# Kernel optimization log

Measured on AMD Instinct MI355X. Metric: run time of the kernel, lower is better.

Reference implementation:

```python
import jax, jax.numpy as jnp
import numpy as np

B, C, Himg, Wimg = 8, 256, 128, 128
KC, VC, HID = 256, 256, 1024


def _conv(x, w, b, pad, groups=1):
    y = jax.lax.conv_general_dilated(
        x, w, (1, 1), [(pad[0], pad[0]), (pad[1], pad[1])],
        dimension_numbers=('NCHW', 'OIHW', 'NCHW'), feature_group_count=groups)
    return y + b[None, :, None, None]


def _ln(x, g, b, eps=1e-5):
    m = x.mean(-1, keepdims=True)
    v = ((x - m) ** 2).mean(-1, keepdims=True)
    return (x - m) / jnp.sqrt(v + eps) * g + b


def setup_inputs() -> dict:
    key = jax.random.key(0)
    ks = jax.random.split(key, 24)
    s = 0.02
    inp = {
        'x': jax.random.normal(ks[0], (B, C, Himg, Wimg), jnp.float32),
        'H': Himg, 'W': Wimg,
        # directional K/Q convs: dir0 kernel (1,3), dir1 kernel (3,1)
        'wk1': s * jax.random.normal(ks[1], (KC, C, 1, 3), jnp.float32),
        'bk1': jnp.zeros((KC,), jnp.float32),
        'wk2': s * jax.random.normal(ks[2], (KC, C, 3, 1), jnp.float32),
        'bk2': jnp.zeros((KC,), jnp.float32),
        'wq1': s * jax.random.normal(ks[3], (KC, C, 1, 3), jnp.float32),
        'bq1': jnp.zeros((KC,), jnp.float32),
        'wq2': s * jax.random.normal(ks[4], (KC, C, 3, 1), jnp.float32),
        'bq2': jnp.zeros((KC,), jnp.float32),
        'wv': s * jax.random.normal(ks[5], (VC, C, 1, 1), jnp.float32),
        'bv': jnp.zeros((VC,), jnp.float32),
        'wr': s * jax.random.normal(ks[6], (C, 2 * VC, 1, 1), jnp.float32),
        'br': jnp.zeros((C,), jnp.float32),
        'g1': jnp.ones((C,), jnp.float32), 'b1': jnp.zeros((C,), jnp.float32),
        'g2': jnp.ones((C,), jnp.float32), 'b2': jnp.zeros((C,), jnp.float32),
        'w_fc1': s * jax.random.normal(ks[7], (HID, C), jnp.float32),
        'b_fc1': jnp.zeros((HID,), jnp.float32),
        'w_dw': s * jax.random.normal(ks[8], (HID, 1, 3, 3), jnp.float32),
        'b_dw': jnp.zeros((HID,), jnp.float32),
        'w_fc2': s * jax.random.normal(ks[9], (C, HID), jnp.float32),
        'b_fc2': jnp.zeros((C,), jnp.float32),
    }
    return inp


def reference(x, H, W, wk1, bk1, wk2, bk2, wq1, bq1, wq2, bq2, wv, bv, wr, br,
              g1, b1, g2, b2, w_fc1, b_fc1, w_dw, b_dw, w_fc2, b_fc2):
    b, c, h, w = x.shape
    N = h * w
    xseq = x.reshape(b, c, N).transpose(0, 2, 1)          # b N c
    n1 = _ln(xseq, g1, b1)
    xn = n1.transpose(0, 2, 1).reshape(b, c, h, w)

    val = _conv(xn, wv, bv, (0, 0)).reshape(b, VC, N)     # b vc n
    attended, maps = [], []
    ctx = None
    for (wk, bk, wq, bq, pad) in [(wk1, bk1, wq1, bq1, (0, 1)),
                                  (wk2, bk2, wq2, bq2, (1, 0))]:
        k = _conv(xn, wk, bk, pad).reshape(b, KC, N)
        q = _conv(xn, wq, bq, pad).reshape(b, KC, N)
        key_s = jax.nn.softmax(k, axis=2)                 # softmax over spatial
        qry_s = jax.nn.softmax(q, axis=1)                 # softmax over channels
        ctx = jnp.einsum('bkn,bvn->bkv', key_s, val)      # O(n) linear attention
        av = jnp.einsum('bkv,bkn->bvn', ctx, qry_s).reshape(b, VC, h, w)
        attended.append(av)
        maps.append(key_s.mean(axis=1).reshape(b, h, w))
    agg = jnp.concatenate(attended, axis=1)               # b 2vc h w
    attn = _conv(agg, wr, br, (0, 0))                     # b c h w
    amap = jnp.stack(maps, axis=0).mean(axis=0)

    tx = xseq + attn.reshape(b, c, N).transpose(0, 2, 1)  # residual
    n2 = _ln(tx, g2, b2)
    h1 = n2 @ w_fc1.T + b_fc1                             # b N 4c
    h1img = h1.transpose(0, 2, 1).reshape(b, HID, h, w)
    dw = _conv(h1img, w_dw, b_dw, (1, 1), groups=HID)
    a = jax.nn.gelu(dw.reshape(b, HID, N).transpose(0, 2, 1), approximate=False)
    ffn = a @ w_fc2.T + b_fc2
    mx = (tx + ffn).transpose(0, 2, 1).reshape(b, c, h, w)
    return (mx, ctx, amap)
```

## Files before the change

kernel.cpp:

```cpp
#include <hip/hip_runtime.h>
#include <hip/hip_bf16.h>

#define B_ 8
#define C_ 256
#define H_ 128
#define W_ 128
#define N_ 16384
#define KC_ 256
#define VC_ 256
#define HID_ 1024

typedef unsigned short ushort_t;
typedef __bf16 bf16x8 __attribute__((ext_vector_type(8)));
typedef float f32x4 __attribute__((ext_vector_type(4)));
typedef ushort_t u16x8 __attribute__((ext_vector_type(8)));

static __device__ __forceinline__ ushort_t f2bu(float f) {
  __hip_bfloat16 h = __float2bfloat16(f);
  return *reinterpret_cast<ushort_t*>(&h);
}
static __device__ __forceinline__ float bu2f(ushort_t u) {
  __hip_bfloat16 h;
  *reinterpret_cast<ushort_t*>(&h) = u;
  return __bfloat162float(h);
}

#define GLD16(gp, lp) __builtin_amdgcn_global_load_lds( \
    (const __attribute__((address_space(1))) void*)(gp), \
    (__attribute__((address_space(3))) void*)(lp), 16, 0, 0)

__global__ __launch_bounds__(256) void pack_all(
    const float* __restrict__ wk1, const float* __restrict__ wk2,
    const float* __restrict__ wq1, const float* __restrict__ wq2,
    const float* __restrict__ wv, const float* __restrict__ wfc1,
    const float* __restrict__ wfc2, const float* __restrict__ wdw,
    const float* __restrict__ bk1, const float* __restrict__ bk2,
    const float* __restrict__ bq1, const float* __restrict__ bq2,
    const float* __restrict__ wr,
    ushort_t* __restrict__ zbuf, float* __restrict__ fzero,
    float* __restrict__ bK, float* __restrict__ bQ, float* __restrict__ wdwT,
    ushort_t* __restrict__ wvp, ushort_t* __restrict__ wfc1p,
    ushort_t* __restrict__ wfc2p, ushort_t* __restrict__ wrp,
    ushort_t* __restrict__ wkkp, ushort_t* __restrict__ wqqp) {
  int idx = blockIdx.x * 256 + threadIdx.x;
  const int MC = KC_ * C_;
  if (idx < 512) {
    zbuf[idx] = 0; fzero[idx] = 0.f;
    bK[idx] = (idx < 256) ? bk1[idx] : bk2[idx - 256];
    bQ[idx] = (idx < 256) ? bq1[idx] : bq2[idx - 256];
    return;
  }
  idx -= 512;
  if (idx < 9216) { int c = idx / 9, t = idx % 9; wdwT[t * HID_ + c] = wdw[idx]; return; }
  idx -= 9216;
  if (idx < VC_ * C_) { wvp[idx] = f2bu(wv[idx]); return; }
  idx -= VC_ * C_;
  if (idx < HID_ * C_) { wfc1p[idx] = f2bu(wfc1[idx]); return; }
  idx -= HID_ * C_;
  if (idx < C_ * HID_) { wfc2p[idx] = f2bu(wfc2[idx]); return; }
  idx -= C_ * HID_;
  if (idx < C_ * 512) { wrp[idx] = f2bu(wr[idx]); return; }
  idx -= C_ * 512;
  if (idx < MC) {
    #pragma unroll
    for (int t = 0; t < 3; ++t) wkkp[t * MC + idx] = f2bu(wk1[idx * 3 + t]);
    return;
  }
  idx -= MC;
  if (idx < MC) {
    #pragma unroll
    for (int t = 0; t < 3; ++t) wkkp[3 * MC + t * MC + idx] = f2bu(wk2[idx * 3 + t]);
    return;
  }
  idx -= MC;
  if (idx < MC) {
    #pragma unroll
    for (int t = 0; t < 3; ++t) wqqp[t * MC + idx] = f2bu(wq1[idx * 3 + t]);
    return;
  }
  idx -= MC;
  if (idx < MC) {
    #pragma unroll
    for (int t = 0; t < 3; ++t) wqqp[3 * MC + t * MC + idx] = f2bu(wq2[idx * 3 + t]);
    return;
  }
}

__global__ __launch_bounds__(256) void ln1t_kernel(const float* __restrict__ x,
    const float* __restrict__ g, const float* __restrict__ beta,
    ushort_t* __restrict__ out) {
  __shared__ float T[256][67];
  __shared__ float st[2][4][64];
  __shared__ float mr[64], rs[64];
  int z = blockIdx.z;
  int n0 = blockIdx.x * 64;
  int t = threadIdx.x;
  const float* xb = x + (size_t)z * C_ * N_;
  #pragma unroll
  for (int j = 0; j < 16; ++j) {
    int e = (j * 256 + t) * 4;
    int c = e >> 6, n = e & 63;
    float4 v = *(const float4*)&xb[(size_t)c * N_ + n0 + n];
    T[c][n] = v.x; T[c][n + 1] = v.y; T[c][n + 2] = v.z; T[c][n + 3] = v.w;
  }
  __syncthreads();
  {
    int n = t & 63, part = t >> 6;
    float s1 = 0.f, s2 = 0.f;
    for (int c = part * 64; c < part * 64 + 64; ++c) { float v = T[c][n]; s1 += v; s2 += v * v; }
    st[0][part][n] = s1; st[1][part][n] = s2;
  }
  __syncthreads();
  if (t < 64) {
    float s1 = st[0][0][t] + st[0][1][t] + st[0][2][t] + st[0][3][t];
    float s2 = st[1][0][t] + st[1][1][t] + st[1][2][t] + st[1][3][t];
    float m = s1 * (1.f / C_);
    float v = s2 * (1.f / C_) - m * m;
    mr[t] = m; rs[t] = rsqrtf(v + 1e-5f);
  }
  __syncthreads();
  {
    int n = t >> 2, cc = (t & 3) * 64;
    float m = mr[n], r = rs[n];
    ushort_t* po = out + (size_t)z * N_ * C_ + (size_t)(n0 + n) * C_ + cc;
    #pragma unroll
    for (int j0 = 0; j0 < 64; j0 += 8) {
      u16x8 o;
      #pragma unroll
      for (int j = 0; j < 8; ++j) {
        int c = cc + j0 + j;
        o[j] = f2bu((T[c][n] - m) * r * g[c] + beta[c]);
      }
      *(u16x8*)(po + j0) = o;
    }
  }
}

__global__ __launch_bounds__(256) void ln2t_kernel(const ushort_t* __restrict__ x,
    const float* __restrict__ g, const float* __restrict__ beta,
    ushort_t* __restrict__ out) {
  __shared__ ushort_t T[256][72];
  __shared__ float st[2][4][64];
  __shared__ float mr[64], rs[64];
  int z = blockIdx.z;
  int n0 = blockIdx.x * 64;
  int t = threadIdx.x;
  const ushort_t* xb = x + (size_t)z * C_ * N_;
  #pragma unroll
  for (int j = 0; j < 8; ++j) {
    int e = (j * 256 + t) * 8;
    int c = e >> 6, n = e & 63;
    *(u16x8*)&T[c][n] = *(const u16x8*)&xb[(size_t)c * N_ + n0 + n];
  }
  __syncthreads();
  {
    int n = t & 63, part = t >> 6;
    float s1 = 0.f, s2 = 0.f;
    for (int c = part * 64; c < part * 64 + 64; ++c) { float v = bu2f(T[c][n]); s1 += v; s2 += v * v; }
    st[0][part][n] = s1; st[1][part][n] = s2;
  }
  __syncthreads();
  if (t < 64) {
    float s1 = st[0][0][t] + st[0][1][t] + st[0][2][t] + st[0][3][t];
    float s2 = st[1][0][t] + st[1][1][t] + st[1][2][t] + st[1][3][t];
    float m = s1 * (1.f / C_);
    float v = s2 * (1.f / C_) - m * m;
    mr[t] = m; rs[t] = rsqrtf(v + 1e-5f);
  }
  __syncthreads();
  {
    int n = t >> 2, cc = (t & 3) * 64;
    float m = mr[n], r = rs[n];
    ushort_t* po = out + (size_t)z * N_ * C_ + (size_t)(n0 + n) * C_ + cc;
    #pragma unroll
    for (int j0 = 0; j0 < 64; j0 += 8) {
      u16x8 o;
      #pragma unroll
      for (int j = 0; j < 8; ++j) {
        int c = cc + j0 + j;
        o[j] = f2bu((bu2f(T[c][n]) - m) * r * g[c] + beta[c]);
      }
      *(u16x8*)(po + j0) = o;
    }
  }
}

template<int TAPS, int DIMSEL, int OMODE, int SPLIT, bool BDUAL>
__global__ __launch_bounds__(256) void mfma_gemm(
    const ushort_t* __restrict__ A, long Abatch, int lda, long Aplane, long Adirstride,
    const ushort_t* __restrict__ B, const ushort_t* __restrict__ B2, long Bbatch, int ldb,
    const float* __restrict__ bias,
    const float* __restrict__ resF, const ushort_t* __restrict__ resB, long Resbatch,
    float* __restrict__ outF, ushort_t* __restrict__ outB, ushort_t* __restrict__ outB2,
    long Outbatch, int ldo, int Ksteps, const ushort_t* __restrict__ zbuf) {
  __shared__ ushort_t sm[17408];
  int tid = threadIdx.x;
  int bx = blockIdx.x, by = blockIdx.y, bz = blockIdx.z;
  if (gridDim.x == 128) bx = ((bx & 7) << 4) | (bx >> 3);
  int b = bz / SPLIT, sK = bz % SPLIT;
  long koff = (long)sK * Ksteps * 64;
  int dsel = (DIMSEL == 3) ? (by < 2 ? 1 : 2) : DIMSEL;
  int m0 = (DIMSEL == 3) ? ((by & 1) * 128) : (by * 128);
  int bofs = (DIMSEL == 3) ? ((by >> 1) * 256) : 0;
  const ushort_t* Ab = A + (size_t)b * Abatch + koff + ((DIMSEL == 3) ? (long)(by >> 1) * Adirstride : 0L);
  const ushort_t* Bb = B + (size_t)b * Bbatch + (BDUAL ? 0 : koff);
  const ushort_t* B2b = BDUAL ? (B2 + (size_t)b * Bbatch) : nullptr;
  int n0 = bx * 128;
  int lane = tid & 63, wid = tid >> 6, wm = wid >> 1, wn = wid & 1;

  f32x4 acc[4][4];
  #pragma unroll
  for (int i = 0; i < 4; i++)
    #pragma unroll
    for (int j = 0; j < 4; j++) acc[i][j] = (f32x4)0.f;

  for (int t = 0; t < TAPS; ++t) {
    if (TAPS == 3 && dsel == 2) {
      if ((bx == 0 && t == 0) || (bx == H_ - 1 && t == 2)) continue;
    }
    const ushort_t* At = Ab + (long)t * Aplane;
    for (int ks = 0; ks < Ksteps; ++ks) {
      int k0 = ks * 64;
      #pragma unroll
      for (int i = 0; i < 4; i++) {
        int s = tid + i * 256;
        int row = s >> 3, pc = s & 7;
        int lc = pc ^ (row & 7);
        const ushort_t* g = At + (long)(m0 + row) * lda + k0 + lc * 8;
        GLD16(g, &sm[s * 8]);
      }
      #pragma unroll
      for (int i = 0; i < 4; i++) {
        int s = tid + i * 256;
        int row = s >> 3, pc = s & 7;
        int lc = pc ^ (row & 7);
        const ushort_t* g;
        if (BDUAL) {
          const ushort_t* Bsel = (ks < Ksteps / 2) ? Bb : B2b;
          int kb = ((ks < Ksteps / 2) ? ks : ks - Ksteps / 2) * 64;
          g = Bsel + (long)(n0 + row) * ldb + kb + lc * 8;
        } else if (TAPS == 3 && dsel == 1) {
          int wpos = row + (t - 1);
          if (0 <= wpos && wpos < W_)
            g = Bb + (long)(n0 + row + (t - 1)) * ldb + k0 + lc * 8;
          else
            g = zbuf;
        } else if (TAPS == 3 && dsel == 2) {
          g = Bb + (long)(n0 + row + (t - 1) * W_) * ldb + k0 + lc * 8;
        } else {
          g = Bb + (long)(n0 + row) * ldb + k0 + lc * 8;
        }
        GLD16(g, &sm[8192 + s * 8]);
      }
      __syncthreads();
      #pragma unroll
      for (int kk = 0; kk < 2; kk++) {
        bf16x8 av[4], bv[4];
        int r16 = lane & 15;
        int sl = (lane >> 4) + kk * 4;
        #pragma unroll
        for (int fm = 0; fm < 4; fm++) {
          int row = wm * 64 + fm * 16 + r16;
          av[fm] = *(const bf16x8*)&sm[row * 64 + ((sl ^ (row & 7)) * 8)];
        }
        #pragma unroll
        for (int fn = 0; fn < 4; fn++) {
          int row = wn * 64 + fn * 16 + r16;
          bv[fn] = *(const bf16x8*)&sm[8192 + row * 64 + ((sl ^ (row & 7)) * 8)];
        }
        #pragma unroll
        for (int fm = 0; fm < 4; fm++)
          #pragma unroll
          for (int fn = 0; fn < 4; fn++)
            acc[fm][fn] = __builtin_amdgcn_mfma_f32_16x16x32_bf16(av[fm], bv[fn], acc[fm][fn], 0, 0, 0);
      }
      __syncthreads();
    }
  }

  int r16 = lane & 15, rq = lane >> 4;
  if (OMODE == 1 || OMODE == 2 || OMODE == 7) {
    ushort_t* obase = (DIMSEL == 3 && blockIdx.y >= 2) ? outB2 : outB;
    ushort_t* ob = obase + (size_t)bz * Outbatch;
    #pragma unroll
    for (int fm = 0; fm < 4; fm++) {
      #pragma unroll
      for (int fn = 0; fn < 4; fn++) {
        int lm = wm * 64 + fm * 16 + rq * 4;
        int ln = wn * 64 + fn * 16 + r16;
        f32x4 a = acc[fm][fn];
        if (OMODE == 2) {
          #pragma unroll
          for (int r = 0; r < 4; r++)
            sm[ln * 136 + lm + r] = f2bu(a[r] + bias[bofs + m0 + lm + r]);
        } else {
          #pragma unroll
          for (int r = 0; r < 4; r++)
            sm[(lm + r) * 136 + ln] = f2bu(a[r] + bias[bofs + m0 + lm + r]);
        }
      }
    }
    __syncthreads();
    int row = tid >> 1, half = (tid & 1) * 64;
    const ushort_t* src = &sm[row * 136 + half];
    if (OMODE == 7) {
      const float* xb = resF + (size_t)bz * Resbatch + (size_t)(m0 + row) * ldo + n0 + half;
      ushort_t* dst = &ob[(size_t)(m0 + row) * ldo + n0 + half];
      #pragma unroll
      for (int j = 0; j < 8; j++) {
        u16x8 v = *(const u16x8*)(src + j * 8);
        float4 x0 = *(const float4*)(xb + j * 8);
        float4 x1 = *(const float4*)(xb + j * 8 + 4);
        u16x8 o;
        o[0] = f2bu(bu2f(v[0]) + x0.x); o[1] = f2bu(bu2f(v[1]) + x0.y);
        o[2] = f2bu(bu2f(v[2]) + x0.z); o[3] = f2bu(bu2f(v[3]) + x0.w);
        o[4] = f2bu(bu2f(v[4]) + x1.x); o[5] = f2bu(bu2f(v[5]) + x1.y);
        o[6] = f2bu(bu2f(v[6]) + x1.z); o[7] = f2bu(bu2f(v[7]) + x1.w);
        *(u16x8*)(dst + j * 8) = o;
      }
    } else {
      ushort_t* dst;
      if (OMODE == 1) dst = &ob[(size_t)(m0 + row) * ldo + n0 + half];
      else            dst = &ob[(size_t)(n0 + row) * ldo + m0 + half];
      #pragma unroll
      for (int j = 0; j < 8; j++)
        *(u16x8*)(dst + j * 8) = *(const u16x8*)(src + j * 8);
    }
  } else {
    #pragma unroll
    for (int fm = 0; fm < 4; fm++) {
      #pragma unroll
      for (int fn = 0; fn < 4; fn++) {
        int mrow = m0 + wm * 64 + fm * 16 + rq * 4;
        int ncol = n0 + wn * 64 + fn * 16 + r16;
        f32x4 a = acc[fm][fn];
        if (OMODE == 6) {
          float* of = outF + (size_t)bz * Outbatch;
          #pragma unroll
          for (int r = 0; r < 4; r++)
            of[(size_t)(mrow + r) * ldo + ncol] = a[r];
        } else if (OMODE == 8) {
          float* of = outF + (size_t)bz * Outbatch;
          const ushort_t* rp = resB + (size_t)bz * Resbatch;
          #pragma unroll
          for (int r = 0; r < 4; r++) {
            size_t o = (size_t)(mrow + r) * ldo + ncol;
            of[o] = a[r] + bias[mrow + r] + bu2f(rp[o]);
          }
        }
      }
    }
  }
}

__global__ __launch_bounds__(256) void softmax_spatial2(ushort_t* __restrict__ p0,
                                                        ushort_t* __restrict__ p1) {
  int r = blockIdx.x;
  ushort_t* p = (r < B_ * KC_) ? (p0 + (size_t)r * N_) : (p1 + (size_t)(r - B_ * KC_) * N_);
  int tid = threadIdx.x;
  __shared__ float red[256];
  u16x8 v[8];
  #pragma unroll
  for (int j = 0; j < 8; j++) v[j] = *(const u16x8*)&p[tid * 8 + j * 2048];
  float mx = -1e30f;
  #pragma unroll
  for (int j = 0; j < 8; j++)
    #pragma unroll
    for (int e = 0; e < 8; e++) mx = fmaxf(mx, bu2f(v[j][e]));
  red[tid] = mx; __syncthreads();
  for (int s = 128; s > 0; s >>= 1) { if (tid < s) red[tid] = fmaxf(red[tid], red[tid + s]); __syncthreads(); }
  mx = red[0]; __syncthreads();
  float sum = 0.f;
  #pragma unroll
  for (int j = 0; j < 8; j++)
    #pragma unroll
    for (int e = 0; e < 8; e++) sum += __expf(bu2f(v[j][e]) - mx);
  red[tid] = sum; __syncthreads();
  for (int s = 128; s > 0; s >>= 1) { if (tid < s) red[tid] += red[tid + s]; __syncthreads(); }
  float inv = 1.f / red[0];
  #pragma unroll
  for (int j = 0; j < 8; j++) {
    u16x8 o;
    #pragma unroll
    for (int e = 0; e < 8; e++) o[e] = f2bu(__expf(bu2f(v[j][e]) - mx) * inv);
    *(u16x8*)&p[tid * 8 + j * 2048] = o;
  }
}

__global__ __launch_bounds__(256) void softmax_channel2(ushort_t* __restrict__ p0,
                                                        ushort_t* __restrict__ p1) {
  int tid = threadIdx.x;
  size_t rowg = (size_t)blockIdx.x * 64 + (tid >> 2);
  int part = tid & 3;
  ushort_t* q = (rowg < (size_t)B_ * N_) ? (p0 + rowg * KC_)
                                         : (p1 + (rowg - (size_t)B_ * N_) * KC_);
  ushort_t* qp = q + part * 64;
  u16x8 v[8];
  #pragma unroll
  for (int j = 0; j < 8; j++) v[j] = *(const u16x8*)&qp[j * 8];
  float mx = -1e30f;
  #pragma unroll
  for (int j = 0; j < 8; j++)
    #pragma unroll
    for (int e = 0; e < 8; e++) mx = fmaxf(mx, bu2f(v[j][e]));
  mx = fmaxf(mx, __shfl_xor(mx, 1));
  mx = fmaxf(mx, __shfl_xor(mx, 2));
  float sum = 0.f;
  #pragma unroll
  for (int j = 0; j < 8; j++)
    #pragma unroll
    for (int e = 0; e < 8; e++) sum += __expf(bu2f(v[j][e]) - mx);
  sum += __shfl_xor(sum, 1);
  sum += __shfl_xor(sum, 2);
  float inv = 1.f / sum;
  #pragma unroll
  for (int j = 0; j < 8; j++) {
    u16x8 o;
    #pragma unroll
    for (int e = 0; e < 8; e++) o[e] = f2bu(__expf(bu2f(v[j][e]) - mx) * inv);
    *(u16x8*)&qp[j * 8] = o;
  }
}

__global__ __launch_bounds__(256) void amap2_kernel(const ushort_t* __restrict__ k0,
    const ushort_t* __restrict__ k1, float* __restrict__ amap) {
  __shared__ float red[256][8];
  int tid = threadIdx.x;
  int ngrp = tid & 63, part = tid >> 6;
  int nblock = blockIdx.x * 512;
  int b = nblock >> 14;
  int n = (nblock & 16383) + ngrp * 8;
  const ushort_t* b0 = k0 + (size_t)b * KC_ * N_ + n;
  const ushort_t* b1 = k1 + (size_t)b * KC_ * N_ + n;
  float s[8];
  #pragma unroll
  for (int j = 0; j < 8; j++) s[j] = 0.f;
  for (int c = part * 64; c < part * 64 + 64; ++c) {
    u16x8 a = *(const u16x8*)&b0[(size_t)c * N_];
    u16x8 d = *(const u16x8*)&b1[(size_t)c * N_];
    #pragma unroll
    for (int j = 0; j < 8; j++) s[j] += bu2f(a[j]) + bu2f(d[j]);
  }
  #pragma unroll
  for (int j = 0; j < 8; j++) red[tid][j] = s[j];
  __syncthreads();
  if (tid < 64) {
    float t[8];
    #pragma unroll
    for (int j = 0; j < 8; j++)
      t[j] = (red[tid][j] + red[tid + 64][j] + red[tid + 128][j] + red[tid + 192][j])
             * (1.f / (2.f * KC_));
    float* dst = amap + (size_t)nblock + tid * 8;
    *(float4*)dst = make_float4(t[0], t[1], t[2], t[3]);
    *(float4*)(dst + 4) = make_float4(t[4], t[5], t[6], t[7]);
  }
}

template<bool F32OUT>
__global__ __launch_bounds__(256) void ctx_reduce(const float* __restrict__ part,
                                                  float* __restrict__ outF,
                                                  ushort_t* __restrict__ outB, int split) {
  int idx = blockIdx.x * 256 + threadIdx.x;
  int b = idx >> 16;
  int r = idx & 65535;
  float s = 0.f;
  for (int k = 0; k < split; k++)
    s += part[((size_t)(b * split + k)) * KC_ * VC_ + r];
  if (F32OUT) outF[idx] = s;
  outB[idx] = f2bu(s);
}

__global__ __launch_bounds__(256) void dwgelu_t(const ushort_t* __restrict__ h1t,
    const float* __restrict__ wdwT, const float* __restrict__ bdw,
    ushort_t* __restrict__ actT) {
  int pix = blockIdx.x * 2 + (threadIdx.x >> 7);
  int c = (threadIdx.x & 127) * 8;
  int h = pix >> 7, w = pix & 127;
  float s[8];
  {
    float4 b0 = *(const float4*)&bdw[c];
    float4 b1 = *(const float4*)&bdw[c + 4];
    s[0]=b0.x; s[1]=b0.y; s[2]=b0.z; s[3]=b0.w;
    s[4]=b1.x; s[5]=b1.y; s[6]=b1.z; s[7]=b1.w;
  }
  #pragma unroll
  for (int di = -1; di <= 1; ++di) {
    int h2 = h + di;
    if ((unsigned)h2 >= H_) continue;
    #pragma unroll
    for (int dj = -1; dj <= 1; ++dj) {
      int w2 = w + dj;
      if ((unsigned)w2 >= W_) continue;
      int tap = (di + 1) * 3 + (dj + 1);
      u16x8 v = *(const u16x8*)&h1t[(size_t)(h2 * W_ + w2) * HID_ + c];
      const float* wp = &wdwT[tap * HID_ + c];
      float4 w0 = *(const float4*)wp, w1 = *(const float4*)(wp + 4);
      s[0] += w0.x * bu2f(v[0]); s[1] += w0.y * bu2f(v[1]);
      s[2] += w0.z * bu2f(v[2]); s[3] += w0.w * bu2f(v[3]);
      s[4] += w1.x * bu2f(v[4]); s[5] += w1.y * bu2f(v[5]);
      s[6] += w1.z * bu2f(v[6]); s[7] += w1.w * bu2f(v[7]);
    }
  }
  u16x8 o;
  #pragma unroll
  for (int j = 0; j < 8; j++) {
    float gl = 0.5f * s[j] * (1.f + erff(s[j] * 0.70710678118654752f));
    o[j] = f2bu(gl);
  }
  *(u16x8*)&actT[(size_t)pix * HID_ + c] = o;
}

extern "C" void kernel_launch(void* const* d_in, const int* in_sizes, int n_in,
                              void* d_out, int out_size, void* d_ws, size_t ws_size,
                              hipStream_t stream) {
  const float* x    = (const float*)d_in[0];
  const float* wk1  = (const float*)d_in[3];
  const float* bk1  = (const float*)d_in[4];
  const float* wk2  = (const float*)d_in[5];
  const float* bk2  = (const float*)d_in[6];
  const float* wq1  = (const float*)d_in[7];
  const float* bq1  = (const float*)d_in[8];
  const float* wq2  = (const float*)d_in[9];
  const float* bq2  = (const float*)d_in[10];
  const float* wv   = (const float*)d_in[11];
  const float* bv   = (const float*)d_in[12];
  const float* wr   = (const float*)d_in[13];
  const float* br   = (const float*)d_in[14];
  const float* g1   = (const float*)d_in[15];
  const float* b1   = (const float*)d_in[16];
  const float* g2   = (const float*)d_in[17];
  const float* b2   = (const float*)d_in[18];
  const float* wfc1 = (const float*)d_in[19];
  const float* bfc1 = (const float*)d_in[20];
  const float* wdw  = (const float*)d_in[21];
  const float* bdw  = (const float*)d_in[22];
  const float* wfc2 = (const float*)d_in[23];
  const float* bfc2 = (const float*)d_in[24];

  const size_t big = (size_t)B_ * C_ * N_;
  const long  CN  = (long)C_ * N_;
  const long  NC2 = (long)N_ * C_;

  uint8_t* w8 = (uint8_t*)d_ws;
  size_t off = 0;
  ushort_t* xnt  = (ushort_t*)(w8 + off); off += 67108864;
  ushort_t* kq   = (ushort_t*)(w8 + off); off += 67108864;
  ushort_t* Mbuf = (ushort_t*)(w8 + off); off += (size_t)B_ * C_ * 512 * 2;
  ushort_t* wkkp = (ushort_t*)(w8 + off); off += 6 * KC_ * C_ * 2;
  ushort_t* wqqp = (ushort_t*)(w8 + off); off += 6 * KC_ * C_ * 2;
  ushort_t* wvp  = (ushort_t*)(w8 + off); off += VC_ * C_ * 2;
  ushort_t* wfc1p= (ushort_t*)(w8 + off); off += HID_ * C_ * 2;
  ushort_t* wfc2p= (ushort_t*)(w8 + off); off += C_ * HID_ * 2;
  float* wdwT    = (float*)(w8 + off);    off += 9 * HID_ * 4;
  float* bK      = (float*)(w8 + off);    off += 512 * 4;
  float* bQ      = (float*)(w8 + off);    off += 512 * 4;
  float* fzero   = (float*)(w8 + off);    off += 512 * 4;
  ushort_t* wrp  = (ushort_t*)(w8 + off); off += C_ * 512 * 2;
  ushort_t* ctx0b= (ushort_t*)(w8 + off); off += (size_t)B_ * KC_ * VC_ * 2;
  ushort_t* ctx1b= (ushort_t*)(w8 + off); off += (size_t)B_ * KC_ * VC_ * 2;
  ushort_t* zbuf = (ushort_t*)(w8 + off); off += 1024;
  float* part    = (float*)(w8 + off);
  size_t need4 = off + (size_t)4 * B_ * KC_ * VC_ * 4;
  size_t need8 = off + (size_t)8 * B_ * KC_ * VC_ * 4;
  int csplit;
  if (ws_size >= need8) csplit = 8;
  else if (ws_size >= need4) csplit = 4;
  else return;

  float* mx_out   = (float*)d_out;
  float* ctx_out  = mx_out + big;
  float* amap_out = ctx_out + (size_t)B_ * KC_ * VC_;

  ushort_t* mxlo = (ushort_t*)d_out;
  ushort_t* mxhi = (ushort_t*)d_out + big;

  ushort_t* txn  = xnt;
  ushort_t* h1t  = kq;
  ushort_t* actT = kq + (size_t)N_ * HID_;

  dim3 blk(256);

  pack_all<<<3878, blk, 0, stream>>>(wk1, wk2, wq1, wq2, wv, wfc1, wfc2, wdw,
                                     bk1, bk2, bq1, bq2, wr,
                                     zbuf, fzero, bK, bQ, wdwT,
                                     wvp, wfc1p, wfc2p, wrp, wkkp, wqqp);

  ln1t_kernel<<<dim3(N_ / 64, 1, B_), blk, 0, stream>>>(x, g1, b1, xnt);

  mfma_gemm<1, 0, 1, 1, false><<<dim3(N_ / 128, VC_ / 128, B_), blk, 0, stream>>>(
      wvp, 0, C_, 0, 0, xnt, nullptr, NC2, C_, bv, nullptr, nullptr, 0,
      nullptr, mxlo, nullptr, (long)VC_ * N_, N_, C_ / 64, zbuf);

  mfma_gemm<3, 3, 1, 1, false><<<dim3(N_ / 128, 4, B_), blk, 0, stream>>>(
      wkkp, 0, C_, (long)KC_ * C_, (long)3 * KC_ * C_, xnt, nullptr, NC2, C_,
      bK, nullptr, nullptr, 0,
      nullptr, kq, mxhi, (long)KC_ * N_, N_, C_ / 64, zbuf);

  softmax_spatial2<<<2 * B_ * KC_, blk, 0, stream>>>(kq, mxhi);
  amap2_kernel<<<B_ * N_ / 512, blk, 0, stream>>>(kq, mxhi, amap_out);

  for (int d = 0; d < 2; ++d) {
    const ushort_t* Ksrc = d ? mxhi : kq;
    if (csplit == 8)
      mfma_gemm<1, 0, 6, 8, false><<<dim3(VC_ / 128, KC_ / 128, B_ * 8), blk, 0, stream>>>(
          Ksrc, (long)KC_ * N_, N_, 0, 0, mxlo, nullptr, (long)VC_ * N_, N_,
          nullptr, nullptr, nullptr, 0,
          part, nullptr, nullptr, (long)KC_ * VC_, VC_, (N_ / 8) / 64, zbuf);
    else
      mfma_gemm<1, 0, 6, 4, false><<<dim3(VC_ / 128, KC_ / 128, B_ * 4), blk, 0, stream>>>(
          Ksrc, (long)KC_ * N_, N_, 0, 0, mxlo, nullptr, (long)VC_ * N_, N_,
          nullptr, nullptr, nullptr, 0,
          part, nullptr, nullptr, (long)KC_ * VC_, VC_, (N_ / 4) / 64, zbuf);
    if (d == 0)
      ctx_reduce<false><<<B_ * KC_ * VC_ / 256, blk, 0, stream>>>(part, nullptr, ctx0b, csplit);
    else
      ctx_reduce<true><<<B_ * KC_ * VC_ / 256, blk, 0, stream>>>(part, ctx_out, ctx1b, csplit);
  }

  mfma_gemm<3, 3, 2, 1, false><<<dim3(N_ / 128, 4, B_), blk, 0, stream>>>(
      wqqp, 0, C_, (long)KC_ * C_, (long)3 * KC_ * C_, xnt, nullptr, NC2, C_,
      bQ, nullptr, nullptr, 0,
      nullptr, kq, mxlo, (long)N_ * KC_, KC_, C_ / 64, zbuf);

  softmax_channel2<<<2 * B_ * N_ / 64, blk, 0, stream>>>(kq, mxlo);

  mfma_gemm<1, 0, 1, 1, false><<<dim3(KC_ / 128, C_ / 128, B_), blk, 0, stream>>>(
      wrp, 0, 512, 0, 0, ctx0b, nullptr, (long)KC_ * VC_, VC_, fzero, nullptr, nullptr, 0,
      nullptr, Mbuf, nullptr, (long)C_ * 512, 512, VC_ / 64, zbuf);
  mfma_gemm<1, 0, 1, 1, false><<<dim3(KC_ / 128, C_ / 128, B_), blk, 0, stream>>>(
      wrp + 256, 0, 512, 0, 0, ctx1b, nullptr, (long)KC_ * VC_, VC_, fzero, nullptr, nullptr, 0,
      nullptr, Mbuf + 256, nullptr, (long)C_ * 512, 512, VC_ / 64, zbuf);

  mfma_gemm<1, 0, 7, 1, true><<<dim3(N_ / 128, C_ / 128, B_), blk, 0, stream>>>(
      Mbuf, (long)C_ * 512, 512, 0, 0, kq, mxlo, (long)N_ * KC_, KC_,
      br, x, nullptr, CN,
      nullptr, mxhi, nullptr, CN, N_, 8, zbuf);

  ln2t_kernel<<<dim3(N_ / 64, 1, B_), blk, 0, stream>>>(mxhi, g2, b2, txn);

  hipMemcpyAsync(part, mxhi + (size_t)7 * CN, (size_t)CN * 2,
                 hipMemcpyDeviceToDevice, stream);

  for (int b = 0; b < B_; ++b) {
    mfma_gemm<1, 0, 2, 1, false><<<dim3(N_ / 128, HID_ / 128, 1), blk, 0, stream>>>(
        wfc1p, 0, C_, 0, 0, txn + (size_t)b * NC2, nullptr, 0, C_,
        bfc1, nullptr, nullptr, 0,
        nullptr, h1t, nullptr, 0, HID_, C_ / 64, zbuf);
    dwgelu_t<<<N_ / 2, blk, 0, stream>>>(h1t, wdwT, bdw, actT);
    const ushort_t* txb = (b == 7) ? (const ushort_t*)part : (mxhi + (size_t)b * CN);
    mfma_gemm<1, 0, 8, 1, false><<<dim3(N_ / 128, C_ / 128, 1), blk, 0, stream>>>(
        wfc2p, 0, HID_, 0, 0, actT, nullptr, 0, HID_,
        bfc2, nullptr, txb, 0,
        mx_out + (size_t)b * CN, nullptr, nullptr, 0, N_, HID_ / 64, zbuf);
  }
}
```

Baseline: 1.481 ms.

## Fuse V projection into directional K conv GEMM and narrow channel softmax rows

Merges the value 1x1 projection into the 3-tap K convolution GEMM launch by adding a DIMSEL=4 mode. The grid grows to six M-blocks, and the last two blocks run a single tap on the V weights, which are laid out right after the K weights, writing to a third output buffer. The change removes one kernel launch and lets the K and V GEMMs share the input tile stream in one grid. Separately, the channel softmax now uses 8 threads per row instead of 4, giving more blocks and interleaved 16-byte accesses. The combined bias buffer and the reused zero buffer replace separate allocations.

```diff
diff --git a/kernel.cpp b/kernel.cpp
--- a/kernel.cpp
+++ b/kernel.cpp
@@ -36,21 +36,25 @@
     const float* __restrict__ wfc2, const float* __restrict__ wdw,
     const float* __restrict__ bk1, const float* __restrict__ bk2,
     const float* __restrict__ bq1, const float* __restrict__ bq2,
-    const float* __restrict__ wr,
-    ushort_t* __restrict__ zbuf, float* __restrict__ fzero,
-    float* __restrict__ bK, float* __restrict__ bQ, float* __restrict__ wdwT,
+    const float* __restrict__ bv, const float* __restrict__ wr,
+    ushort_t* __restrict__ zbuf,
+    float* __restrict__ bKV, float* __restrict__ bQ, float* __restrict__ wdwT,
     ushort_t* __restrict__ wvp, ushort_t* __restrict__ wfc1p,
     ushort_t* __restrict__ wfc2p, ushort_t* __restrict__ wrp,
     ushort_t* __restrict__ wkkp, ushort_t* __restrict__ wqqp) {
   int idx = blockIdx.x * 256 + threadIdx.x;
   const int MC = KC_ * C_;
   if (idx < 512) {
-    zbuf[idx] = 0; fzero[idx] = 0.f;
-    bK[idx] = (idx < 256) ? bk1[idx] : bk2[idx - 256];
+    zbuf[idx] = 0;
     bQ[idx] = (idx < 256) ? bq1[idx] : bq2[idx - 256];
     return;
   }
   idx -= 512;
+  if (idx < 768) {
+    bKV[idx] = (idx < 256) ? bk1[idx] : (idx < 512 ? bk2[idx - 256] : bv[idx - 512]);
+    return;
+  }
+  idx -= 768;
   if (idx < 9216) { int c = idx / 9, t = idx % 9; wdwT[t * HID_ + c] = wdw[idx]; return; }
   idx -= 9216;
   if (idx < VC_ * C_) { wvp[idx] = f2bu(wv[idx]); return; }
@@ -192,6 +196,7 @@
     const float* __restrict__ bias,
     const float* __restrict__ resF, const ushort_t* __restrict__ resB, long Resbatch,
     float* __restrict__ outF, ushort_t* __restrict__ outB, ushort_t* __restrict__ outB2,
+    ushort_t* __restrict__ outB3,
     long Outbatch, int ldo, int Ksteps, const ushort_t* __restrict__ zbuf) {
   __shared__ ushort_t sm[17408];
   int tid = threadIdx.x;
@@ -199,10 +204,13 @@
   if (gridDim.x == 128) bx = ((bx & 7) << 4) | (bx >> 3);
   int b = bz / SPLIT, sK = bz % SPLIT;
   long koff = (long)sK * Ksteps * 64;
-  int dsel = (DIMSEL == 3) ? (by < 2 ? 1 : 2) : DIMSEL;
-  int m0 = (DIMSEL == 3) ? ((by & 1) * 128) : (by * 128);
-  int bofs = (DIMSEL == 3) ? ((by >> 1) * 256) : 0;
-  const ushort_t* Ab = A + (size_t)b * Abatch + koff + ((DIMSEL == 3) ? (long)(by >> 1) * Adirstride : 0L);
+  int dsel = (DIMSEL == 3) ? (by < 2 ? 1 : 2)
+           : (DIMSEL == 4) ? (by < 2 ? 1 : (by < 4 ? 2 : 0))
+           : DIMSEL;
+  int m0 = (DIMSEL == 3 || DIMSEL == 4) ? ((by & 1) * 128) : (by * 128);
+  int bofs = (DIMSEL == 3 || DIMSEL == 4) ? ((by >> 1) * 256) : 0;
+  const ushort_t* Ab = A + (size_t)b * Abatch + koff
+      + ((DIMSEL == 3 || DIMSEL == 4) ? (long)(by >> 1) * Adirstride : 0L);
   const ushort_t* Bb = B + (size_t)b * Bbatch + (BDUAL ? 0 : koff);
   const ushort_t* B2b = BDUAL ? (B2 + (size_t)b * Bbatch) : nullptr;
   int n0 = bx * 128;
@@ -218,7 +226,8 @@
     if (TAPS == 3 && dsel == 2) {
       if ((bx == 0 && t == 0) || (bx == H_ - 1 && t == 2)) continue;
     }
-    const ushort_t* At = Ab + (long)t * Aplane;
+    if (DIMSEL == 4 && dsel == 0 && t != 1) continue;
+    const ushort_t* At = Ab + ((DIMSEL == 4 && dsel == 0) ? 0L : (long)t * Aplane);
     for (int ks = 0; ks < Ksteps; ++ks) {
       int k0 = ks * 64;
       #pragma unroll
@@ -280,7 +289,11 @@
 
   int r16 = lane & 15, rq = lane >> 4;
   if (OMODE == 1 || OMODE == 2 || OMODE == 7) {
-    ushort_t* obase = (DIMSEL == 3 && blockIdx.y >= 2) ? outB2 : outB;
+    ushort_t* obase;
+    if (DIMSEL == 3 || DIMSEL == 4)
+      obase = (blockIdx.y >= 4) ? outB3 : (blockIdx.y >= 2 ? outB2 : outB);
+    else
+      obase = outB;
     ushort_t* ob = obase + (size_t)bz * Outbatch;
     #pragma unroll
     for (int fm = 0; fm < 4; fm++) {
@@ -390,35 +403,36 @@
 __global__ __launch_bounds__(256) void softmax_channel2(ushort_t* __restrict__ p0,
                                                         ushort_t* __restrict__ p1) {
   int tid = threadIdx.x;
-  size_t rowg = (size_t)blockIdx.x * 64 + (tid >> 2);
-  int part = tid & 3;
+  size_t rowg = (size_t)blockIdx.x * 32 + (tid >> 3);
+  int part = tid & 7;
   ushort_t* q = (rowg < (size_t)B_ * N_) ? (p0 + rowg * KC_)
                                          : (p1 + (rowg - (size_t)B_ * N_) * KC_);
-  ushort_t* qp = q + part * 64;
-  u16x8 v[8];
-  #pragma unroll
-  for (int j = 0; j < 8; j++) v[j] = *(const u16x8*)&qp[j * 8];
+  u16x8 v[4];
+  #pragma unroll
+  for (int j = 0; j < 4; j++) v[j] = *(const u16x8*)&q[part * 8 + j * 64];
   float mx = -1e30f;
   #pragma unroll
-  for (int j = 0; j < 8; j++)
+  for (int j = 0; j < 4; j++)
     #pragma unroll
     for (int e = 0; e < 8; e++) mx = fmaxf(mx, bu2f(v[j][e]));
   mx = fmaxf(mx, __shfl_xor(mx, 1));
   mx = fmaxf(mx, __shfl_xor(mx, 2));
+  mx = fmaxf(mx, __shfl_xor(mx, 4));
   float sum = 0.f;
   #pragma unroll
-  for (int j = 0; j < 8; j++)
+  for (int j = 0; j < 4; j++)
     #pragma unroll
     for (int e = 0; e < 8; e++) sum += __expf(bu2f(v[j][e]) - mx);
   sum += __shfl_xor(sum, 1);
   sum += __shfl_xor(sum, 2);
+  sum += __shfl_xor(sum, 4);
   float inv = 1.f / sum;
   #pragma unroll
-  for (int j = 0; j < 8; j++) {
+  for (int j = 0; j < 4; j++) {
     u16x8 o;
     #pragma unroll
     for (int e = 0; e < 8; e++) o[e] = f2bu(__expf(bu2f(v[j][e]) - mx) * inv);
-    *(u16x8*)&qp[j * 8] = o;
+    *(u16x8*)&q[part * 8 + j * 64] = o;
   }
 }
 
@@ -540,21 +554,21 @@
   const size_t big = (size_t)B_ * C_ * N_;
   const long  CN  = (long)C_ * N_;
   const long  NC2 = (long)N_ * C_;
+  const int   MC  = KC_ * C_;
 
   uint8_t* w8 = (uint8_t*)d_ws;
   size_t off = 0;
   ushort_t* xnt  = (ushort_t*)(w8 + off); off += 67108864;
   ushort_t* kq   = (ushort_t*)(w8 + off); off += 67108864;
   ushort_t* Mbuf = (ushort_t*)(w8 + off); off += (size_t)B_ * C_ * 512 * 2;
-  ushort_t* wkkp = (ushort_t*)(w8 + off); off += 6 * KC_ * C_ * 2;
-  ushort_t* wqqp = (ushort_t*)(w8 + off); off += 6 * KC_ * C_ * 2;
-  ushort_t* wvp  = (ushort_t*)(w8 + off); off += VC_ * C_ * 2;
+  ushort_t* wkkp = (ushort_t*)(w8 + off); off += 6 * MC * 2;
+  ushort_t* wvp  = (ushort_t*)(w8 + off); off += MC * 2;
+  ushort_t* wqqp = (ushort_t*)(w8 + off); off += 6 * MC * 2;
   ushort_t* wfc1p= (ushort_t*)(w8 + off); off += HID_ * C_ * 2;
   ushort_t* wfc2p= (ushort_t*)(w8 + off); off += C_ * HID_ * 2;
   float* wdwT    = (float*)(w8 + off);    off += 9 * HID_ * 4;
-  float* bK      = (float*)(w8 + off);    off += 512 * 4;
+  float* bKV     = (float*)(w8 + off);    off += 768 * 4;
   float* bQ      = (float*)(w8 + off);    off += 512 * 4;
-  float* fzero   = (float*)(w8 + off);    off += 512 * 4;
   ushort_t* wrp  = (ushort_t*)(w8 + off); off += C_ * 512 * 2;
   ushort_t* ctx0b= (ushort_t*)(w8 + off); off += (size_t)B_ * KC_ * VC_ * 2;
   ushort_t* ctx1b= (ushort_t*)(w8 + off); off += (size_t)B_ * KC_ * VC_ * 2;
@@ -566,6 +580,7 @@
   if (ws_size >= need8) csplit = 8;
   else if (ws_size >= need4) csplit = 4;
   else return;
+  const float* fzero = (const float*)zbuf;
 
   float* mx_out   = (float*)d_out;
   float* ctx_out  = mx_out + big;
@@ -580,21 +595,17 @@
 
   dim3 blk(256);
 
-  pack_all<<<3878, blk, 0, stream>>>(wk1, wk2, wq1, wq2, wv, wfc1, wfc2, wdw,
-                                     bk1, bk2, bq1, bq2, wr,
-                                     zbuf, fzero, bK, bQ, wdwT,
+  pack_all<<<3881, blk, 0, stream>>>(wk1, wk2, wq1, wq2, wv, wfc1, wfc2, wdw,
+                                     bk1, bk2, bq1, bq2, bv, wr,
+                                     zbuf, bKV, bQ, wdwT,
                                      wvp, wfc1p, wfc2p, wrp, wkkp, wqqp);
 
   ln1t_kernel<<<dim3(N_ / 64, 1, B_), blk, 0, stream>>>(x, g1, b1, xnt);
 
-  mfma_gemm<1, 0, 1, 1, false><<<dim3(N_ / 128, VC_ / 128, B_), blk, 0, stream>>>(
-      wvp, 0, C_, 0, 0, xnt, nullptr, NC2, C_, bv, nullptr, nullptr, 0,
-      nullptr, mxlo, nullptr, (long)VC_ * N_, N_, C_ / 64, zbuf);
-
-  mfma_gemm<3, 3, 1, 1, false><<<dim3(N_ / 128, 4, B_), blk, 0, stream>>>(
-      wkkp, 0, C_, (long)KC_ * C_, (long)3 * KC_ * C_, xnt, nullptr, NC2, C_,
-      bK, nullptr, nullptr, 0,
-      nullptr, kq, mxhi, (long)KC_ * N_, N_, C_ / 64, zbuf);
+  mfma_gemm<3, 4, 1, 1, false><<<dim3(N_ / 128, 6, B_), blk, 0, stream>>>(
+      wkkp, 0, C_, (long)MC, (long)3 * MC, xnt, nullptr, NC2, C_,
+      bKV, nullptr, nullptr, 0,
+      nullptr, kq, mxhi, mxlo, (long)KC_ * N_, N_, C_ / 64, zbuf);
 
   softmax_spatial2<<<2 * B_ * KC_, blk, 0, stream>>>(kq, mxhi);
   amap2_kernel<<<B_ * N_ / 512, blk, 0, stream>>>(kq, mxhi, amap_out);
@@ -605,12 +616,12 @@
       mfma_gemm<1, 0, 6, 8, false><<<dim3(VC_ / 128, KC_ / 128, B_ * 8), blk, 0, stream>>>(
           Ksrc, (long)KC_ * N_, N_, 0, 0, mxlo, nullptr, (long)VC_ * N_, N_,
           nullptr, nullptr, nullptr, 0,
-          part, nullptr, nullptr, (long)KC_ * VC_, VC_, (N_ / 8) / 64, zbuf);
+          part, nullptr, nullptr, nullptr, (long)KC_ * VC_, VC_, (N_ / 8) / 64, zbuf);
     else
       mfma_gemm<1, 0, 6, 4, false><<<dim3(VC_ / 128, KC_ / 128, B_ * 4), blk, 0, stream>>>(
           Ksrc, (long)KC_ * N_, N_, 0, 0, mxlo, nullptr, (long)VC_ * N_, N_,
           nullptr, nullptr, nullptr, 0,
-          part, nullptr, nullptr, (long)KC_ * VC_, VC_, (N_ / 4) / 64, zbuf);
+          part, nullptr, nullptr, nullptr, (long)KC_ * VC_, VC_, (N_ / 4) / 64, zbuf);
     if (d == 0)
       ctx_reduce<false><<<B_ * KC_ * VC_ / 256, blk, 0, stream>>>(part, nullptr, ctx0b, csplit);
     else
@@ -618,23 +629,23 @@
   }
 
   mfma_gemm<3, 3, 2, 1, false><<<dim3(N_ / 128, 4, B_), blk, 0, stream>>>(
-      wqqp, 0, C_, (long)KC_ * C_, (long)3 * KC_ * C_, xnt, nullptr, NC2, C_,
+      wqqp, 0, C_, (long)MC, (long)3 * MC, xnt, nullptr, NC2, C_,
       bQ, nullptr, nullptr, 0,
-      nullptr, kq, mxlo, (long)N_ * KC_, KC_, C_ / 64, zbuf);
-
-  softmax_channel2<<<2 * B_ * N_ / 64, blk, 0, stream>>>(kq, mxlo);
+      nullptr, kq, mxlo, nullptr, (long)N_ * KC_, KC_, C_ / 64, zbuf);
+
+  softmax_channel2<<<2 * B_ * N_ / 32, blk, 0, stream>>>(kq, mxlo);
 
   mfma_gemm<1, 0, 1, 1, false><<<dim3(KC_ / 128, C_ / 128, B_), blk, 0, stream>>>(
       wrp, 0, 512, 0, 0, ctx0b, nullptr, (long)KC_ * VC_, VC_, fzero, nullptr, nullptr, 0,
-      nullptr, Mbuf, nullptr, (long)C_ * 512, 512, VC_ / 64, zbuf);
+      nullptr, Mbuf, nullptr, nullptr, (long)C_ * 512, 512, VC_ / 64, zbuf);
   mfma_gemm<1, 0, 1, 1, false><<<dim3(KC_ / 128, C_ / 128, B_), blk, 0, stream>>>(
       wrp + 256, 0, 512, 0, 0, ctx1b, nullptr, (long)KC_ * VC_, VC_, fzero, nullptr, nullptr, 0,
-      nullptr, Mbuf + 256, nullptr, (long)C_ * 512, 512, VC_ / 64, zbuf);
+      nullptr, Mbuf + 256, nullptr, nullptr, (long)C_ * 512, 512, VC_ / 64, zbuf);
 
   mfma_gemm<1, 0, 7, 1, true><<<dim3(N_ / 128, C_ / 128, B_), blk, 0, stream>>>(
       Mbuf, (long)C_ * 512, 512, 0, 0, kq, mxlo, (long)N_ * KC_, KC_,
       br, x, nullptr, CN,
-      nullptr, mxhi, nullptr, CN, N_, 8, zbuf);
+      nullptr, mxhi, nullptr, nullptr, CN, N_, 8, zbuf);
 
   ln2t_kernel<<<dim3(N_ / 64, 1, B_), blk, 0, stream>>>(mxhi, g2, b2, txn);
 
@@ -645,12 +656,12 @@
     mfma_gemm<1, 0, 2, 1, false><<<dim3(N_ / 128, HID_ / 128, 1), blk, 0, stream>>>(
         wfc1p, 0, C_, 0, 0, txn + (size_t)b * NC2, nullptr, 0, C_,
         bfc1, nullptr, nullptr, 0,
-        nullptr, h1t, nullptr, 0, HID_, C_ / 64, zbuf);
+        nullptr, h1t, nullptr, nullptr, 0, HID_, C_ / 64, zbuf);
     dwgelu_t<<<N_ / 2, blk, 0, stream>>>(h1t, wdwT, bdw, actT);
     const ushort_t* txb = (b == 7) ? (const ushort_t*)part : (mxhi + (size_t)b * CN);
     mfma_gemm<1, 0, 8, 1, false><<<dim3(N_ / 128, C_ / 128, 1), blk, 0, stream>>>(
         wfc2p, 0, HID_, 0, 0, actT, nullptr, 0, HID_,
         bfc2, nullptr, txb, 0,
-        mx_out + (size_t)b * CN, nullptr, nullptr, 0, N_, HID_ / 64, zbuf);
-  }
-}
+        mx_out + (size_t)b * CN, nullptr, nullptr, nullptr, 0, N_, HID_ / 64, zbuf);
+  }
+}
```

Result: faster. 1.437 ms (-3.0%).
